# Performance work log

Hardware: AMD Instinct MI355X
Metric: run time of the kernel (lower is better)

Reference implementation:

```python
import jax, jax.numpy as jnp
import numpy as np

N = 16384      # total nodes
B = 8          # graphs in batch
NPG = N // B   # nodes per graph
E = 262144     # edges
IN, HID, OUT = 128, 256, 128
ICP_ITERS = 10


def setup_inputs():
    key = jax.random.key(0)
    ks = jax.random.split(key, 12)
    x = jax.random.normal(ks[0], (N, IN), jnp.float32)
    # random edges kept within each graph (offsets per graph)
    src = jax.random.randint(ks[1], (E,), 0, NPG, dtype=jnp.int32)
    dst = jax.random.randint(ks[2], (E,), 0, NPG, dtype=jnp.int32)
    goff = (jnp.arange(E, dtype=jnp.int32) % B) * NPG
    edge_index = jnp.stack([src + goff, dst + goff], 0)
    pos = jax.random.normal(ks[3], (N, 3), jnp.float32)
    batch = jnp.repeat(jnp.arange(B, dtype=jnp.int32), NPG)
    def lin(k, fi, fo):
        return jax.random.normal(k, (fi, fo), jnp.float32) * (fi ** -0.5)
    return dict(
        x=x, edge_index=edge_index, pos=pos, batch=batch,
        W1=lin(ks[4], IN, HID),  b1=jnp.zeros((HID,), jnp.float32),
        W2=lin(ks[5], HID, HID), b2=jnp.zeros((HID,), jnp.float32),
        W3=lin(ks[6], HID, OUT), b3=jnp.zeros((OUT,), jnp.float32),
        Wt=lin(ks[7], OUT, 3),   bt=jnp.zeros((3,), jnp.float32),
    )


def gcn_conv(x, W, b, row, col, n):
    # GCNConv: symmetric norm with self loops; messages flow row->col
    xw = x @ W
    loop = jnp.arange(n, dtype=row.dtype)
    r = jnp.concatenate([row, loop])
    c = jnp.concatenate([col, loop])
    deg = jax.ops.segment_sum(jnp.ones_like(c, dtype=xw.dtype), c, num_segments=n)
    dinv = jnp.where(deg > 0, jax.lax.rsqrt(jnp.maximum(deg, 1e-12)), 0.0)
    norm = dinv[r] * dinv[c]
    out = jax.ops.segment_sum(xw[r] * norm[:, None], c, num_segments=n)
    return out + b


def pdist2(a, b):
    # squared pairwise distances [n,m]
    return (jnp.sum(a * a, -1)[:, None] + jnp.sum(b * b, -1)[None, :]
            - 2.0 * (a @ b.T))


def icp_align(src, tgt):
    # fixed-iteration batched ICP (Kabsch/SVD per iteration)
    for _ in range(ICP_ITERS):
        d = pdist2(jax.lax.stop_gradient(src), jax.lax.stop_gradient(tgt))
        idx = jnp.argmin(d, axis=1)
        corr = tgt[idx]
        cs = jnp.mean(src, 0)
        cc = jnp.mean(corr, 0)
        H = (src - cs).T @ (corr - cc)  # [3,3]
        U, S, Vt = jnp.linalg.svd(H, full_matrices=False)
        sign = jnp.sign(jnp.linalg.det(Vt.T @ U.T))
        D = jnp.stack([jnp.ones_like(sign), jnp.ones_like(sign), sign])
        R = (Vt.T * D[None, :]) @ U.T
        t = cc - R @ cs
        src = src @ R.T + t
    return src


def chamfer(a, b):
    d = pdist2(jax.lax.stop_gradient(a), jax.lax.stop_gradient(b))
    ia = jnp.argmin(d, 1)
    ib = jnp.argmin(d, 0)
    d1 = jnp.mean(jnp.sum((a - b[ia]) ** 2, -1))
    d2 = jnp.mean(jnp.sum((b - a[ib]) ** 2, -1))
    return d1 + d2


def reference(x, edge_index, pos, batch, W1, b1, W2, b2, W3, b3, Wt, bt):
    n = x.shape[0]
    row, col = edge_index[0], edge_index[1]
    h = jax.nn.relu(gcn_conv(x, W1, b1, row, col, n))
    h = jax.nn.relu(gcn_conv(h, W2, b2, row, col, n))
    h = gcn_conv(h, W3, b3, row, col, n)
    pos_offset = h @ Wt + bt
    tpos = pos + pos_offset
    nb = int(batch[-1]) + 1          # sorted, equal-size graphs
    npg = n // nb
    src = tpos.reshape(nb, npg, 3)
    tgt = pos.reshape(nb, npg, 3)
    aligned = jax.vmap(icp_align)(src, tgt)
    loss = jnp.mean(jax.vmap(chamfer)(aligned, tgt))
    return h, aligned.reshape(n, 3), loss
```

## Files before the change

### kernel.cpp

```cpp
#include <hip/hip_runtime.h>
#include <math.h>

#define N_NODES 16384
#define B_GRAPHS 8
#define NPG_     2048
#define E_EDGES  262144
#define F_IN  128
#define F_HID 256
#define F_OUT 128
#define ICP_IT 10
#define NN_BPG 32

typedef __attribute__((ext_vector_type(8))) short bf16x8;
typedef __attribute__((ext_vector_type(4))) float f32x4;

__device__ __forceinline__ float b2f(unsigned short u) {
    union { unsigned int u; float f; } v; v.u = ((unsigned int)u) << 16; return v.f;
}
__device__ __forceinline__ unsigned short f2b(float f) {
    union { float f; unsigned int u; } v; v.f = f;
    unsigned int r = v.u + 0x7FFFu + ((v.u >> 16) & 1u);
    return (unsigned short)(r >> 16);
}
__device__ __forceinline__ int swz32(int i) {
    return (i & ~31) | ((i & 31) ^ ((i >> 5) & 31));
}
__device__ __forceinline__ void st_agent(float* p, float v) {
    __hip_atomic_store(p, v, __ATOMIC_RELAXED, __HIP_MEMORY_SCOPE_AGENT);
}
__device__ __forceinline__ float ld_agent(const float* p) {
    return __hip_atomic_load(p, __ATOMIC_RELAXED, __HIP_MEMORY_SCOPE_AGENT);
}
__device__ __forceinline__ int ld_agent_i(const int* p) {
    return __hip_atomic_load(p, __ATOMIC_RELAXED, __HIP_MEMORY_SCOPE_AGENT);
}

__global__ __launch_bounds__(256) void k_prep(
    const float* __restrict__ x, unsigned short* __restrict__ xb,
    const float* __restrict__ W1, const float* __restrict__ W2, const float* __restrict__ W3,
    unsigned short* __restrict__ W1b, unsigned short* __restrict__ W2b, unsigned short* __restrict__ W3b,
    int* __restrict__ counts, int* __restrict__ ctrs)
{
    const int b = blockIdx.x, tid = threadIdx.x;
    if (b < 2048) {
        int i = b * 256 + tid;
        float4 v = ((const float4*)x)[i];
        uint2 o;
        o.x = (unsigned int)f2b(v.x) | ((unsigned int)f2b(v.y) << 16);
        o.y = (unsigned int)f2b(v.z) | ((unsigned int)f2b(v.w) << 16);
        ((uint2*)xb)[i] = o;
    } else if (b < 2176) {
        int idx = (b - 2048) * 256 + tid;
        int k = idx >> 8, n = idx & 255;
        W1b[n * 128 + k] = f2b(W1[idx]);
    } else if (b < 2432) {
        int idx = (b - 2176) * 256 + tid;
        int k = idx >> 8, n = idx & 255;
        W2b[n * 256 + k] = f2b(W2[idx]);
    } else if (b < 2560) {
        int idx = (b - 2432) * 256 + tid;
        int k = idx >> 7, n = idx & 127;
        W3b[n * 256 + k] = f2b(W3[idx]);
    } else if (b < 2576) {
        int i = (b - 2560) * 256 + tid;
        ((int4*)counts)[i] = make_int4(0, 0, 0, 0);
    } else {
        ctrs[tid] = 0;
    }
}

__global__ void k_count(const int* __restrict__ col, int* __restrict__ counts) {
    int e = blockIdx.x * 256 + threadIdx.x;
    if (e < E_EDGES) atomicAdd(&counts[col[e]], 1);
}

__global__ __launch_bounds__(1024) void k_scan(const int* __restrict__ counts,
        int* __restrict__ offs, int* __restrict__ cursor, float* __restrict__ dinv)
{
    __shared__ int wtot[16];
    const int t = threadIdx.x;
    const int base = t * 16;
    int local[16];
    int s = 0;
#pragma unroll
    for (int i = 0; i < 16; i++) { local[i] = counts[base + i]; s += local[i]; }
    const int lane = t & 63, w = t >> 6;
    int inc = s;
    for (int o = 1; o < 64; o <<= 1) {
        int v = __shfl_up(inc, o);
        if (lane >= o) inc += v;
    }
    if (lane == 63) wtot[w] = inc;
    __syncthreads();
    if (t < 16) {
        int v = wtot[t];
        for (int o = 1; o < 16; o <<= 1) {
            int u = __shfl_up(v, o);
            if (t >= o) v += u;
        }
        wtot[t] = v;
    }
    __syncthreads();
    int run = (w > 0 ? wtot[w - 1] : 0) + (inc - s);
#pragma unroll
    for (int i = 0; i < 16; i++) {
        offs[base + i]   = run;
        cursor[base + i] = run;
        dinv[base + i]   = rsqrtf((float)(local[i] + 1));
        run += local[i];
    }
    if (t == 1023) offs[N_NODES] = run;
}

__global__ void k_scatter(const int* __restrict__ row, const int* __restrict__ col,
        int* __restrict__ cursor, const float* __restrict__ dinv,
        int* __restrict__ srcid, float* __restrict__ normv)
{
    int e = blockIdx.x * 256 + threadIdx.x;
    if (e >= E_EDGES) return;
    int r = row[e], c = col[e];
    int p = atomicAdd(&cursor[c], 1);
    srcid[p] = r;
    normv[p] = dinv[r] * dinv[c];
}

template<int W, int OUTF, int FUSET>
__global__ __launch_bounds__(128) void k_agg(const unsigned short* __restrict__ X,
        void* __restrict__ Y,
        const int* __restrict__ offs, const int* __restrict__ srcid,
        const float* __restrict__ normv, const float* __restrict__ dinv,
        const float* __restrict__ bias, int relu,
        const float* __restrict__ Wt, const float* __restrict__ bt,
        const float* __restrict__ pos, float* __restrict__ tposO)
{
    constexpr int NPB = (W == 128) ? 2 : 1;
    constexpr int W2 = W / 2;
    const int local = (NPB == 2) ? (threadIdx.x >> 6) : 0;
    const int n = blockIdx.x * NPB + local;
    const int j = (NPB == 2) ? (threadIdx.x & 63) : threadIdx.x;
    const unsigned int* Xu = (const unsigned int*)X;
    float di = dinv[n];
    float w0 = di * di;
    unsigned int v = Xu[(size_t)n * W2 + j];
    float a0 = b2f((unsigned short)v) * w0;
    float a1 = b2f((unsigned short)(v >> 16)) * w0;
    int p = offs[n];
    const int p1 = offs[n + 1];
    for (; p + 3 < p1; p += 4) {
        int s0i = srcid[p], s1i = srcid[p + 1], s2i = srcid[p + 2], s3i = srcid[p + 3];
        float n0 = normv[p], n1 = normv[p + 1], n2 = normv[p + 2], n3 = normv[p + 3];
        unsigned int v0 = Xu[(size_t)s0i * W2 + j];
        unsigned int v1 = Xu[(size_t)s1i * W2 + j];
        unsigned int v2 = Xu[(size_t)s2i * W2 + j];
        unsigned int v3 = Xu[(size_t)s3i * W2 + j];
        a0 = fmaf(b2f((unsigned short)v0), n0, a0);
        a1 = fmaf(b2f((unsigned short)(v0 >> 16)), n0, a1);
        a0 = fmaf(b2f((unsigned short)v1), n1, a0);
        a1 = fmaf(b2f((unsigned short)(v1 >> 16)), n1, a1);
        a0 = fmaf(b2f((unsigned short)v2), n2, a0);
        a1 = fmaf(b2f((unsigned short)(v2 >> 16)), n2, a1);
        a0 = fmaf(b2f((unsigned short)v3), n3, a0);
        a1 = fmaf(b2f((unsigned short)(v3 >> 16)), n3, a1);
    }
    for (; p < p1; ++p) {
        unsigned int va = Xu[(size_t)srcid[p] * W2 + j]; float na = normv[p];
        a0 = fmaf(b2f((unsigned short)va), na, a0);
        a1 = fmaf(b2f((unsigned short)(va >> 16)), na, a1);
    }
    if (bias) { a0 += bias[2 * j]; a1 += bias[2 * j + 1]; }
    if (relu) { a0 = fmaxf(a0, 0.f); a1 = fmaxf(a1, 0.f); }
    if (OUTF) {
        float* Yf = (float*)Y;
        Yf[(size_t)n * W + 2 * j]     = a0;
        Yf[(size_t)n * W + 2 * j + 1] = a1;
    } else {
        ((unsigned int*)Y)[(size_t)n * W2 + j] =
            (unsigned int)f2b(a0) | ((unsigned int)f2b(a1) << 16);
    }
    if (FUSET) {
        float wt0 = Wt[6 * j + 0], wt1 = Wt[6 * j + 1], wt2 = Wt[6 * j + 2];
        float wt3 = Wt[6 * j + 3], wt4 = Wt[6 * j + 4], wt5 = Wt[6 * j + 5];
        float s0 = a0 * wt0 + a1 * wt3;
        float s1 = a0 * wt1 + a1 * wt4;
        float s2 = a0 * wt2 + a1 * wt5;
        for (int o = 32; o > 0; o >>= 1) {
            s0 += __shfl_down(s0, o);
            s1 += __shfl_down(s1, o);
            s2 += __shfl_down(s2, o);
        }
        if (j == 0) {
            tposO[n * 3 + 0] = pos[n * 3 + 0] + s0 + bt[0];
            tposO[n * 3 + 1] = pos[n * 3 + 1] + s1 + bt[1];
            tposO[n * 3 + 2] = pos[n * 3 + 2] + s2 + bt[2];
        }
    }
}

__global__ __launch_bounds__(256) void k_gemm_bf16(
    const unsigned short* __restrict__ A,
    const unsigned short* __restrict__ Bt,
    const float* __restrict__ bias, unsigned short* __restrict__ C,
    int M, int N, int K, int relu)
{
    __shared__ __align__(16) unsigned short As[128 * 64];
    __shared__ __align__(16) unsigned short Bs[64 * 64];
    const int tid  = threadIdx.x;
    const int lane = tid & 63;
    const int wave = tid >> 6;
    const int bm = blockIdx.y * 128, bn = blockIdx.x * 64;
    const int wm = (wave >> 1) * 64, wn = (wave & 1) * 32;
    f32x4 acc[4][2];
#pragma unroll
    for (int mf = 0; mf < 4; mf++)
#pragma unroll
        for (int nf = 0; nf < 2; nf++) acc[mf][nf] = (f32x4){0.f, 0.f, 0.f, 0.f};

    for (int k0 = 0; k0 < K; k0 += 64) {
#pragma unroll
        for (int i = 0; i < 4; i++) {
            int idx = i * 256 + tid;
            int m = idx >> 3, slot = idx & 7;
            const unsigned short* src = A + (size_t)(bm + m) * K + k0 + ((slot ^ (m & 7)) << 3);
            __builtin_amdgcn_global_load_lds(
                (const __attribute__((address_space(1))) unsigned int*)src,
                (__attribute__((address_space(3))) unsigned int*)(As + (size_t)i * 2048 + wave * 512),
                16, 0, 0);
        }
#pragma unroll
        for (int i = 0; i < 2; i++) {
            int idx = i * 256 + tid;
            int n = idx >> 3, slot = idx & 7;
            const unsigned short* src = Bt + (size_t)(bn + n) * K + k0 + ((slot ^ (n & 7)) << 3);
            __builtin_amdgcn_global_load_lds(
                (const __attribute__((address_space(1))) unsigned int*)src,
                (__attribute__((address_space(3))) unsigned int*)(Bs + (size_t)i * 2048 + wave * 512),
                16, 0, 0);
        }
        __syncthreads();
        bf16x8 af[4][2], bfr[2][2];
        const int qd = lane >> 4;
#pragma unroll
        for (int s = 0; s < 2; s++) {
#pragma unroll
            for (int mf = 0; mf < 4; mf++) {
                int m = wm + mf * 16 + (lane & 15);
                int slot = (s * 4 + qd) ^ (m & 7);
                af[mf][s] = *(const bf16x8*)(As + m * 64 + slot * 8);
            }
#pragma unroll
            for (int nf = 0; nf < 2; nf++) {
                int n = wn + nf * 16 + (lane & 15);
                int slot = (s * 4 + qd) ^ (n & 7);
                bfr[nf][s] = *(const bf16x8*)(Bs + n * 64 + slot * 8);
            }
        }
#pragma unroll
        for (int s = 0; s < 2; s++)
#pragma unroll
            for (int mf = 0; mf < 4; mf++)
#pragma unroll
                for (int nf = 0; nf < 2; nf++)
                    acc[mf][nf] = __builtin_amdgcn_mfma_f32_16x16x32_bf16(
                        af[mf][s], bfr[nf][s], acc[mf][nf], 0, 0, 0);
        __syncthreads();
    }
#pragma unroll
    for (int nf = 0; nf < 2; nf++) {
        int col = bn + wn + nf * 16 + (lane & 15);
        float bv = bias ? bias[col] : 0.f;
#pragma unroll
        for (int mf = 0; mf < 4; mf++) {
#pragma unroll
            for (int r = 0; r < 4; r++) {
                int row = bm + wm + mf * 16 + (lane >> 4) * 4 + r;
                float v = acc[mf][nf][r] + bv;
                if (relu) v = fmaxf(v, 0.f);
                C[(size_t)row * N + col] = f2b(v);
            }
        }
    }
}

__global__ __launch_bounds__(512) void k_icp_all(
    const float* __restrict__ tpos, const float* __restrict__ pos,
    float* __restrict__ partials,
    float* __restrict__ chpart,
    int* __restrict__ ctrs,
    float* __restrict__ out_aligned, float* __restrict__ out_loss)
{
    const int g = blockIdx.x >> 5, blk = blockIdx.x & 31;
    const int tid = threadIdx.x;
    const int wave = tid >> 6, lane = tid & 63;
    __shared__ float4 tq[NPG_];
    __shared__ __align__(16) unsigned char scratch[NPG_ * 16];
    float* sm_d = (float*)scratch;
    unsigned short* sm_i = (unsigned short*)(scratch + 64 * 65 * 4);
    float4* al = (float4*)scratch;
    __shared__ float mom[15][33];
    __shared__ float ssx[64], ssy[64], ssz[64];
    __shared__ float wred[16][2];
    __shared__ float Tsh[12];
    __shared__ double sdl[15];
    __shared__ int lastFlag;

    for (int i = tid; i < NPG_; i += 512) {
        const float* p = &pos[(size_t)(g * NPG_ + i) * 3];
        float qx = p[0], qy = p[1], qz = p[2];
        tq[swz32(i)] = make_float4(qx, qy, qz, fmaf(qx, qx, fmaf(qy, qy, qz * qz)));
    }
    if (tid < 12) Tsh[tid] = (tid == 0 || tid == 4 || tid == 8) ? 1.f : 0.f;
    float Px[8], Py[8], Pz[8];
#pragma unroll
    for (int u = 0; u < 8; u++) {
        int n = g * NPG_ + blk * 64 + wave * 8 + u;
        Px[u] = tpos[n * 3 + 0]; Py[u] = tpos[n * 3 + 1]; Pz[u] = tpos[n * 3 + 2];
    }
    double Td[12];
    if (tid == 0) {
#pragma unroll
        for (int k = 0; k < 12; k++) Td[k] = (k == 0 || k == 4 || k == 8) ? 1.0 : 0.0;
    }
    __syncthreads();

    for (int iter = 0; iter < ICP_IT; ++iter) {
        const int bufbase = (iter & 1) * 256;
        float Tf[12];
#pragma unroll
        for (int k = 0; k < 12; k++) Tf[k] = Tsh[k];
        float Sx[8], Sy[8], Sz[8], Tx[8], Ty[8], Tz[8], bd[8];
        int bi[8];
#pragma unroll
        for (int u = 0; u < 8; u++) {
            float X = Tf[0] * Px[u] + Tf[1] * Py[u] + Tf[2] * Pz[u] + Tf[9];
            float Y = Tf[3] * Px[u] + Tf[4] * Py[u] + Tf[5] * Pz[u] + Tf[10];
            float Z = Tf[6] * Px[u] + Tf[7] * Py[u] + Tf[8] * Pz[u] + Tf[11];
            Sx[u] = X; Sy[u] = Y; Sz[u] = Z;
            Tx[u] = -2.f * X; Ty[u] = -2.f * Y; Tz[u] = -2.f * Z;
            bd[u] = 1e30f; bi[u] = lane * 32;
        }
        const int qbase = lane * 32;
        for (int j = 0; j < 32; j++) {
            float4 t4 = tq[qbase + (j ^ (lane & 31))];
            int idx = qbase + j;
#pragma unroll
            for (int u = 0; u < 8; u++) {
                float d = fmaf(Tx[u], t4.x, fmaf(Ty[u], t4.y, fmaf(Tz[u], t4.z, t4.w)));
                if (d < bd[u]) { bd[u] = d; bi[u] = idx; }
            }
        }
#pragma unroll
        for (int u = 0; u < 8; u++) {
            int rowoff = (wave * 8 + u) * 65;
            sm_d[rowoff + lane] = bd[u];
            sm_i[rowoff + lane] = (unsigned short)bi[u];
            if (lane == u) { ssx[wave * 8 + u] = Sx[u]; ssy[wave * 8 + u] = Sy[u]; ssz[wave * 8 + u] = Sz[u]; }
        }
        __syncthreads();
        if (tid < 64) {
            const int s = tid;
            float best = sm_d[s * 65];
            int ib = sm_i[s * 65];
            for (int r = 1; r < 64; r++) {
                float dd = sm_d[s * 65 + r];
                int ii = sm_i[s * 65 + r];
                if (dd < best) { best = dd; ib = ii; }
            }
            float4 c = tq[swz32(ib)];
            float X = ssx[s], Y = ssy[s], Z = ssz[s];
            float vals[15] = { X, Y, Z, c.x, c.y, c.z,
                               X * c.x, X * c.y, X * c.z,
                               Y * c.x, Y * c.y, Y * c.z,
                               Z * c.x, Z * c.y, Z * c.z };
#pragma unroll
            for (int k = 0; k < 15; k++) {
                float v = vals[k];
                for (int o = 32; o > 0; o >>= 1) v += __shfl_down(v, o);
                if (tid == 0) st_agent(&partials[((size_t)bufbase + blockIdx.x) * 16 + k], v);
            }
        }
        __syncthreads();
        if (tid == 0) {
            atomicAdd(&ctrs[g * 16], 1);
            const int target = 32 * (iter + 1);
            while (ld_agent_i(&ctrs[g * 16]) < target) __builtin_amdgcn_s_sleep(8);
        }
        __syncthreads();
        if (tid < 480) {
            int kk = tid >> 5, bb = tid & 31;
            mom[kk][bb] = ld_agent(&partials[((size_t)bufbase + g * 32 + bb) * 16 + kk]);
        }
        __syncthreads();
        if (tid < 15) {
            double acc = 0;
            for (int b = 0; b < NN_BPG; b++) acc += (double)mom[tid][b];
            sdl[tid] = acc;
        }
        __syncthreads();
        if (tid == 0) {
            double sd[15];
#pragma unroll
            for (int k = 0; k < 15; k++) sd[k] = sdl[k];
            const double n = (double)NPG_;
            const double rin = 1.0 / (double)NPG_;
            double cs0 = sd[0] * rin, cs1 = sd[1] * rin, cs2 = sd[2] * rin;
            double cc0 = sd[3] * rin, cc1 = sd[4] * rin, cc2 = sd[5] * rin;
            float H[3][3];
            H[0][0] = (float)(sd[6]  - n * cs0 * cc0); H[0][1] = (float)(sd[7]  - n * cs0 * cc1); H[0][2] = (float)(sd[8]  - n * cs0 * cc2);
            H[1][0] = (float)(sd[9]  - n * cs1 * cc0); H[1][1] = (float)(sd[10] - n * cs1 * cc1); H[1][2] = (float)(sd[11] - n * cs1 * cc2);
            H[2][0] = (float)(sd[12] - n * cs2 * cc0); H[2][1] = (float)(sd[13] - n * cs2 * cc1); H[2][2] = (float)(sd[14] - n * cs2 * cc2);
            double R[3][3];
            float fn = 1e-30f;
            for (int i = 0; i < 3; i++) for (int j2 = 0; j2 < 3; j2++) fn += H[i][j2] * H[i][j2];
            float sc = rsqrtf(fn);
            float Xm[3][3];
            for (int i = 0; i < 3; i++) for (int j2 = 0; j2 < 3; j2++) Xm[i][j2] = H[i][j2] * sc;
            float dX = Xm[0][0] * (Xm[1][1]*Xm[2][2] - Xm[1][2]*Xm[2][1])
                     - Xm[0][1] * (Xm[1][0]*Xm[2][2] - Xm[1][2]*Xm[2][0])
                     + Xm[0][2] * (Xm[1][0]*Xm[2][1] - Xm[1][1]*Xm[2][0]);
            if (dX > 1e-4f) {
                for (int itn = 0; itn < 24; ++itn) {
                    float C00 = Xm[1][1]*Xm[2][2] - Xm[1][2]*Xm[2][1];
                    float C01 = Xm[1][2]*Xm[2][0] - Xm[1][0]*Xm[2][2];
                    float C02 = Xm[1][0]*Xm[2][1] - Xm[1][1]*Xm[2][0];
                    float C10 = Xm[2][1]*Xm[0][2] - Xm[2][2]*Xm[0][1];
                    float C11 = Xm[2][2]*Xm[0][0] - Xm[2][0]*Xm[0][2];
                    float C12 = Xm[2][0]*Xm[0][1] - Xm[2][1]*Xm[0][0];
                    float C20 = Xm[0][1]*Xm[1][2] - Xm[0][2]*Xm[1][1];
                    float C21 = Xm[0][2]*Xm[1][0] - Xm[0][0]*Xm[1][2];
                    float C22 = Xm[0][0]*Xm[1][1] - Xm[0][1]*Xm[1][0];
                    float det = Xm[0][0]*C00 + Xm[0][1]*C01 + Xm[0][2]*C02;
                    if (fabsf(det) < 1e-30f) break;
                    float rd = 0.5f / det;
                    Xm[0][0] = 0.5f*Xm[0][0] + C00*rd; Xm[0][1] = 0.5f*Xm[0][1] + C01*rd; Xm[0][2] = 0.5f*Xm[0][2] + C02*rd;
                    Xm[1][0] = 0.5f*Xm[1][0] + C10*rd; Xm[1][1] = 0.5f*Xm[1][1] + C11*rd; Xm[1][2] = 0.5f*Xm[1][2] + C12*rd;
                    Xm[2][0] = 0.5f*Xm[2][0] + C20*rd; Xm[2][1] = 0.5f*Xm[2][1] + C21*rd; Xm[2][2] = 0.5f*Xm[2][2] + C22*rd;
                }
                for (int i = 0; i < 3; i++) for (int j2 = 0; j2 < 3; j2++) R[i][j2] = (double)Xm[j2][i];
            } else {
                float A[3][3], V[3][3] = {{1,0,0},{0,1,0},{0,0,1}};
                for (int i = 0; i < 3; i++)
                    for (int j2 = 0; j2 < 3; j2++)
                        A[i][j2] = H[0][i] * H[0][j2] + H[1][i] * H[1][j2] + H[2][i] * H[2][j2];
                for (int sweep = 0; sweep < 8; ++sweep) {
                    for (int p = 0; p < 2; p++) for (int q = p + 1; q < 3; q++) {
                        float apq = A[p][q];
                        if (fabsf(apq) < 1e-30f) continue;
                        float theta = (A[q][q] - A[p][p]) / (2.f * apq);
                        float t = copysignf(1.f, theta) / (fabsf(theta) + sqrtf(theta * theta + 1.f));
                        float c = 1.f / sqrtf(t * t + 1.f);
                        float s = t * c;
                        for (int k = 0; k < 3; k++) { float akp = A[k][p], akq = A[k][q]; A[k][p] = c*akp - s*akq; A[k][q] = s*akp + c*akq; }
                        for (int k = 0; k < 3; k++) { float apk = A[p][k], aqk = A[q][k]; A[p][k] = c*apk - s*aqk; A[q][k] = s*apk + c*aqk; }
                        for (int k = 0; k < 3; k++) { float vkp = V[k][p], vkq = V[k][q]; V[k][p] = c*vkp - s*vkq; V[k][q] = s*vkp + c*vkq; }
                    }
                }
                float lam[3] = { A[0][0], A[1][1], A[2][2] };
                int ord[3] = { 0, 1, 2 };
                if (lam[ord[1]] > lam[ord[0]]) { int t0 = ord[0]; ord[0] = ord[1]; ord[1] = t0; }
                if (lam[ord[2]] > lam[ord[0]]) { int t0 = ord[0]; ord[0] = ord[2]; ord[2] = t0; }
                if (lam[ord[2]] > lam[ord[1]]) { int t0 = ord[1]; ord[1] = ord[2]; ord[2] = t0; }
                float vc[3][3], uc[3][3];
                for (int i = 0; i < 3; i++) { vc[i][0] = V[0][ord[i]]; vc[i][1] = V[1][ord[i]]; vc[i][2] = V[2][ord[i]]; }
                for (int i = 0; i < 3; i++) {
                    float u0 = H[0][0]*vc[i][0] + H[0][1]*vc[i][1] + H[0][2]*vc[i][2];
                    float u1 = H[1][0]*vc[i][0] + H[1][1]*vc[i][1] + H[1][2]*vc[i][2];
                    float u2 = H[2][0]*vc[i][0] + H[2][1]*vc[i][1] + H[2][2]*vc[i][2];
                    for (int j2 = 0; j2 < i; j2++) {
                        float dp = u0*uc[j2][0] + u1*uc[j2][1] + u2*uc[j2][2];
                        u0 -= dp*uc[j2][0]; u1 -= dp*uc[j2][1]; u2 -= dp*uc[j2][2];
                    }
                    float nn2 = sqrtf(u0*u0 + u1*u1 + u2*u2);
                    if (nn2 > 1e-12f) { uc[i][0] = u0/nn2; uc[i][1] = u1/nn2; uc[i][2] = u2/nn2; }
                    else if (i == 2) {
                        uc[2][0] = uc[0][1]*uc[1][2] - uc[0][2]*uc[1][1];
                        uc[2][1] = uc[0][2]*uc[1][0] - uc[0][0]*uc[1][2];
                        uc[2][2] = uc[0][0]*uc[1][1] - uc[0][1]*uc[1][0];
                    } else if (i == 1) {
                        float a0 = (fabsf(uc[0][0]) < 0.9f) ? 1.f : 0.f, a1 = 1.f - a0, a2 = 0.f;
                        float dp = a0*uc[0][0] + a1*uc[0][1] + a2*uc[0][2];
                        a0 -= dp*uc[0][0]; a1 -= dp*uc[0][1]; a2 -= dp*uc[0][2];
                        float nn3 = sqrtf(a0*a0 + a1*a1 + a2*a2);
                        uc[1][0] = a0/nn3; uc[1][1] = a1/nn3; uc[1][2] = a2/nn3;
                    } else { uc[0][0] = 1; uc[0][1] = 0; uc[0][2] = 0; }
                }
                float detU = uc[0][0]*(uc[1][1]*uc[2][2] - uc[1][2]*uc[2][1])
                           - uc[0][1]*(uc[1][0]*uc[2][2] - uc[1][2]*uc[2][0])
                           + uc[0][2]*(uc[1][0]*uc[2][1] - uc[1][1]*uc[2][0]);
                float detV = vc[0][0]*(vc[1][1]*vc[2][2] - vc[1][2]*vc[2][1])
                           - vc[0][1]*(vc[1][0]*vc[2][2] - vc[1][2]*vc[2][0])
                           + vc[0][2]*(vc[1][0]*vc[2][1] - vc[1][1]*vc[2][0]);
                float sgn = (detU * detV < 0.f) ? -1.f : 1.f;
                for (int i = 0; i < 3; i++)
                    for (int j2 = 0; j2 < 3; j2++)
                        R[i][j2] = (double)(vc[0][i]*uc[0][j2] + vc[1][i]*uc[1][j2] + sgn * vc[2][i]*uc[2][j2]);
            }
            double tr0 = cc0 - (R[0][0]*cs0 + R[0][1]*cs1 + R[0][2]*cs2);
            double tr1 = cc1 - (R[1][0]*cs0 + R[1][1]*cs1 + R[1][2]*cs2);
            double tr2 = cc2 - (R[2][0]*cs0 + R[2][1]*cs1 + R[2][2]*cs2);
            double An[12];
            for (int i = 0; i < 3; i++)
                for (int j2 = 0; j2 < 3; j2++)
                    An[i*3+j2] = R[i][0]*Td[0*3+j2] + R[i][1]*Td[1*3+j2] + R[i][2]*Td[2*3+j2];
            An[9]  = R[0][0]*Td[9] + R[0][1]*Td[10] + R[0][2]*Td[11] + tr0;
            An[10] = R[1][0]*Td[9] + R[1][1]*Td[10] + R[1][2]*Td[11] + tr1;
            An[11] = R[2][0]*Td[9] + R[2][1]*Td[10] + R[2][2]*Td[11] + tr2;
#pragma unroll
            for (int k = 0; k < 12; k++) { Td[k] = An[k]; Tsh[k] = (float)An[k]; }
        }
        __syncthreads();
    }

    {
        float Tf[12];
#pragma unroll
        for (int k = 0; k < 12; k++) Tf[k] = Tsh[k];
        __syncthreads();
        for (int i = tid; i < NPG_; i += 512) {
            const float* q = &tpos[(size_t)(g * NPG_ + i) * 3];
            float X = Tf[0] * q[0] + Tf[1] * q[1] + Tf[2] * q[2] + Tf[9];
            float Y = Tf[3] * q[0] + Tf[4] * q[1] + Tf[5] * q[2] + Tf[10];
            float Z = Tf[6] * q[0] + Tf[7] * q[1] + Tf[8] * q[2] + Tf[11];
            al[swz32(i)] = make_float4(X, Y, Z, fmaf(X, X, fmaf(Y, Y, Z * Z)));
            if (blk == 0) {
                out_aligned[(size_t)(g * NPG_ + i) * 3 + 0] = X;
                out_aligned[(size_t)(g * NPG_ + i) * 3 + 1] = Y;
                out_aligned[(size_t)(g * NPG_ + i) * 3 + 2] = Z;
            }
        }
        __syncthreads();
        float Ax[8], Ay[8], Az[8], Aw[8], Qx[8], Qy[8], Qz[8], Qw[8], d1[8], d2[8];
#pragma unroll
        for (int u = 0; u < 8; u++) {
            int s = swz32(blk * 64 + wave * 8 + u);
            float4 a4 = al[s]; float4 p4 = tq[s];
            Ax[u] = -2.f * a4.x; Ay[u] = -2.f * a4.y; Az[u] = -2.f * a4.z; Aw[u] = a4.w;
            Qx[u] = -2.f * p4.x; Qy[u] = -2.f * p4.y; Qz[u] = -2.f * p4.z; Qw[u] = p4.w;
            d1[u] = 1e30f; d2[u] = 1e30f;
        }
        const int qbase = lane * 32;
        for (int j = 0; j < 32; j++) {
            int s = qbase + (j ^ (lane & 31));
            float4 t4 = tq[s];
            float4 b4 = al[s];
#pragma unroll
            for (int u = 0; u < 8; u++) {
                d1[u] = fminf(d1[u], fmaf(Ax[u], t4.x, fmaf(Ay[u], t4.y, fmaf(Az[u], t4.z, t4.w))));
                d2[u] = fminf(d2[u], fmaf(Qx[u], b4.x, fmaf(Qy[u], b4.y, fmaf(Qz[u], b4.z, b4.w))));
            }
        }
        float s1 = 0.f, s2 = 0.f;
#pragma unroll
        for (int u = 0; u < 8; u++) {
            float a = d1[u], b = d2[u];
            for (int o = 32; o > 0; o >>= 1) {
                a = fminf(a, __shfl_down(a, o));
                b = fminf(b, __shfl_down(b, o));
            }
            s1 += a + Aw[u];
            s2 += b + Qw[u];
        }
        if (lane == 0) { wred[wave][0] = s1; wred[wave][1] = s2; }
        __syncthreads();
        if (tid == 0) {
            float t1 = 0.f, t2 = 0.f;
#pragma unroll
            for (int w = 0; w < 8; w++) { t1 += wred[w][0]; t2 += wred[w][1]; }
            st_agent(&chpart[blockIdx.x * 2 + 0], t1);
            st_agent(&chpart[blockIdx.x * 2 + 1], t2);
        }
        __syncthreads();
        if (tid == 0) {
            int old = atomicAdd(&ctrs[128], 1);
            lastFlag = (old == (int)gridDim.x - 1) ? 1 : 0;
        }
        __syncthreads();
        if (!lastFlag) return;
        float v1 = 0.f, v2 = 0.f;
        if (tid < 256) {
            v1 = ld_agent(&chpart[tid * 2 + 0]);
            v2 = ld_agent(&chpart[tid * 2 + 1]);
        }
        for (int o = 32; o > 0; o >>= 1) {
            v1 += __shfl_down(v1, o);
            v2 += __shfl_down(v2, o);
        }
        if (lane == 0 && wave < 4) { wred[wave][0] = v1; wred[wave][1] = v2; }
        __syncthreads();
        if (tid == 0) {
            float tot = 0.f;
#pragma unroll
            for (int w = 0; w < 4; w++) tot += wred[w][0] + wred[w][1];
            out_loss[0] = tot / (float)(NPG_ * B_GRAPHS);
        }
    }
}

extern "C" void kernel_launch(void* const* d_in, const int* in_sizes, int n_in,
                              void* d_out, int out_size, void* d_ws, size_t ws_size,
                              hipStream_t stream)
{
    (void)in_sizes; (void)n_in; (void)out_size; (void)ws_size;
    const float* x   = (const float*)d_in[0];
    const int*   ei  = (const int*)d_in[1];
    const float* pos = (const float*)d_in[2];
    const float* W1 = (const float*)d_in[4];
    const float* b1 = (const float*)d_in[5];
    const float* W2 = (const float*)d_in[6];
    const float* b2 = (const float*)d_in[7];
    const float* W3 = (const float*)d_in[8];
    const float* b3 = (const float*)d_in[9];
    const float* Wt = (const float*)d_in[10];
    const float* bt = (const float*)d_in[11];
    const int* row = ei;
    const int* col = ei + E_EDGES;

    char* wsb = (char*)d_ws;
    size_t off_b = 0;
    auto alloc = [&](size_t bytes) -> void* {
        void* p = wsb + off_b;
        off_b = (off_b + bytes + 255) & ~(size_t)255;
        return p;
    };
    int*    counts   = (int*)alloc((size_t)N_NODES * 4);
    int*    offs     = (int*)alloc((size_t)(N_NODES + 1) * 4);
    int*    cursor   = (int*)alloc((size_t)N_NODES * 4);
    int*    srcid    = (int*)alloc((size_t)E_EDGES * 4);
    float*  normv    = (float*)alloc((size_t)E_EDGES * 4);
    float*  dinv     = (float*)alloc((size_t)N_NODES * 4);
    unsigned short* xb  = (unsigned short*)alloc((size_t)N_NODES * F_IN * 2);
    unsigned short* W1b = (unsigned short*)alloc((size_t)F_IN * F_HID * 2);
    unsigned short* W2b = (unsigned short*)alloc((size_t)F_HID * F_HID * 2);
    unsigned short* W3b = (unsigned short*)alloc((size_t)F_HID * F_OUT * 2);
    unsigned short* bufA = (unsigned short*)alloc((size_t)N_NODES * F_HID * 2);
    unsigned short* bufB = (unsigned short*)alloc((size_t)N_NODES * F_HID * 2);
    unsigned short* bufC = (unsigned short*)alloc((size_t)N_NODES * F_HID * 2);
    float*  tpos     = (float*)alloc((size_t)N_NODES * 3 * 4);
    float*  partials = (float*)alloc((size_t)2 * 256 * 16 * 4);
    int*    ctrs     = (int*)alloc((size_t)256 * 4);
    float*  chpart   = (float*)alloc((size_t)256 * 2 * 4);

    float* out_h       = (float*)d_out;
    float* out_aligned = out_h + (size_t)N_NODES * F_OUT;
    float* out_loss    = out_aligned + (size_t)N_NODES * 3;

    k_prep<<<2577, 256, 0, stream>>>(x, xb, W1, W2, W3, W1b, W2b, W3b, counts, ctrs);
    k_count<<<E_EDGES / 256, 256, 0, stream>>>(col, counts);
    k_scan<<<1, 1024, 0, stream>>>(counts, offs, cursor, dinv);
    k_scatter<<<E_EDGES / 256, 256, 0, stream>>>(row, col, cursor, dinv, srcid, normv);

    k_agg<F_IN, 0, 0><<<N_NODES / 2, 128, 0, stream>>>(xb, bufA, offs, srcid, normv, dinv,
            nullptr, 0, nullptr, nullptr, nullptr, nullptr);
    {
        dim3 grid(F_HID / 64, N_NODES / 128);
        k_gemm_bf16<<<grid, 256, 0, stream>>>(bufA, W1b, b1, bufB, N_NODES, F_HID, F_IN, 1);
    }
    {
        dim3 grid(F_HID / 64, N_NODES / 128);
        k_gemm_bf16<<<grid, 256, 0, stream>>>(bufB, W2b, nullptr, bufC, N_NODES, F_HID, F_HID, 0);
    }
    k_agg<F_HID, 0, 0><<<N_NODES, 128, 0, stream>>>(bufC, bufA, offs, srcid, normv, dinv,
            b2, 1, nullptr, nullptr, nullptr, nullptr);
    {
        dim3 grid(F_OUT / 64, N_NODES / 128);
        k_gemm_bf16<<<grid, 256, 0, stream>>>(bufA, W3b, nullptr, bufB, N_NODES, F_OUT, F_HID, 0);
    }
    k_agg<F_OUT, 1, 1><<<N_NODES / 2, 128, 0, stream>>>(bufB, out_h, offs, srcid, normv, dinv,
            b3, 0, Wt, bt, pos, tpos);

    k_icp_all<<<B_GRAPHS * NN_BPG, 512, 0, stream>>>(tpos, pos, partials, chpart, ctrs,
            out_aligned, out_loss);
}
```

Baseline: 330.8 us.

## Split ICP over twice as many smaller blocks and fold edge count into prep

The ICP kernel now runs 512 blocks of 256 threads (64 blocks per graph, 32 source points per block) instead of 256 blocks of 512 threads. The aim is to spread the per-iteration nearest-neighbour search over more compute units, at the cost of a larger cross-block reduction and a grid barrier with more participants each iteration. Separately, the edge-degree counting kernel is merged into the prep kernel, and counts are zeroed by a memset so the standalone count launch goes away. The fused version relies on the memset finishing before prep runs.

```diff
diff --git a/kernel.cpp b/kernel.cpp
--- a/kernel.cpp
+++ b/kernel.cpp
@@ -9,7 +9,6 @@
 #define F_HID 256
 #define F_OUT 128
 #define ICP_IT 10
-#define NN_BPG 32
 
 typedef __attribute__((ext_vector_type(8))) short bf16x8;
 typedef __attribute__((ext_vector_type(4))) float f32x4;
@@ -39,7 +38,7 @@
     const float* __restrict__ x, unsigned short* __restrict__ xb,
     const float* __restrict__ W1, const float* __restrict__ W2, const float* __restrict__ W3,
     unsigned short* __restrict__ W1b, unsigned short* __restrict__ W2b, unsigned short* __restrict__ W3b,
-    int* __restrict__ counts, int* __restrict__ ctrs)
+    const int* __restrict__ col, int* __restrict__ counts, int* __restrict__ ctrs)
 {
     const int b = blockIdx.x, tid = threadIdx.x;
     if (b < 2048) {
@@ -61,17 +60,12 @@
         int idx = (b - 2432) * 256 + tid;
         int k = idx >> 7, n = idx & 127;
         W3b[n * 256 + k] = f2b(W3[idx]);
-    } else if (b < 2576) {
-        int i = (b - 2560) * 256 + tid;
-        ((int4*)counts)[i] = make_int4(0, 0, 0, 0);
+    } else if (b < 3584) {
+        int e = (b - 2560) * 256 + tid;
+        atomicAdd(&counts[col[e]], 1);
     } else {
         ctrs[tid] = 0;
     }
-}
-
-__global__ void k_count(const int* __restrict__ col, int* __restrict__ counts) {
-    int e = blockIdx.x * 256 + threadIdx.x;
-    if (e < E_EDGES) atomicAdd(&counts[col[e]], 1);
 }
 
 __global__ __launch_bounds__(1024) void k_scan(const int* __restrict__ counts,
@@ -281,29 +275,29 @@
     }
 }
 
-__global__ __launch_bounds__(512) void k_icp_all(
+__global__ __launch_bounds__(256, 2) void k_icp_all(
     const float* __restrict__ tpos, const float* __restrict__ pos,
     float* __restrict__ partials,
     float* __restrict__ chpart,
     int* __restrict__ ctrs,
     float* __restrict__ out_aligned, float* __restrict__ out_loss)
 {
-    const int g = blockIdx.x >> 5, blk = blockIdx.x & 31;
+    const int g = blockIdx.x >> 6, blk = blockIdx.x & 63;
     const int tid = threadIdx.x;
     const int wave = tid >> 6, lane = tid & 63;
     __shared__ float4 tq[NPG_];
     __shared__ __align__(16) unsigned char scratch[NPG_ * 16];
     float* sm_d = (float*)scratch;
-    unsigned short* sm_i = (unsigned short*)(scratch + 64 * 65 * 4);
+    unsigned short* sm_i = (unsigned short*)(scratch + 32 * 65 * 4);
     float4* al = (float4*)scratch;
-    __shared__ float mom[15][33];
-    __shared__ float ssx[64], ssy[64], ssz[64];
-    __shared__ float wred[16][2];
+    __shared__ float mom[15][66];
+    __shared__ float crs[32][9];
+    __shared__ float wred[4][2];
     __shared__ float Tsh[12];
     __shared__ double sdl[15];
     __shared__ int lastFlag;
 
-    for (int i = tid; i < NPG_; i += 512) {
+    for (int i = tid; i < NPG_; i += 256) {
         const float* p = &pos[(size_t)(g * NPG_ + i) * 3];
         float qx = p[0], qy = p[1], qz = p[2];
         tq[swz32(i)] = make_float4(qx, qy, qz, fmaf(qx, qx, fmaf(qy, qy, qz * qz)));
@@ -312,7 +306,7 @@
     float Px[8], Py[8], Pz[8];
 #pragma unroll
     for (int u = 0; u < 8; u++) {
-        int n = g * NPG_ + blk * 64 + wave * 8 + u;
+        int n = g * NPG_ + blk * 32 + wave * 8 + u;
         Px[u] = tpos[n * 3 + 0]; Py[u] = tpos[n * 3 + 1]; Pz[u] = tpos[n * 3 + 2];
     }
     double Td[12];
@@ -323,7 +317,7 @@
     __syncthreads();
 
     for (int iter = 0; iter < ICP_IT; ++iter) {
-        const int bufbase = (iter & 1) * 256;
+        const int bufbase = (iter & 1) * 512;
         float Tf[12];
 #pragma unroll
         for (int k = 0; k < 12; k++) Tf[k] = Tsh[k];
@@ -350,49 +344,56 @@
         }
 #pragma unroll
         for (int u = 0; u < 8; u++) {
-            int rowoff = (wave * 8 + u) * 65;
-            sm_d[rowoff + lane] = bd[u];
-            sm_i[rowoff + lane] = (unsigned short)bi[u];
-            if (lane == u) { ssx[wave * 8 + u] = Sx[u]; ssy[wave * 8 + u] = Sy[u]; ssz[wave * 8 + u] = Sz[u]; }
-        }
-        __syncthreads();
-        if (tid < 64) {
-            const int s = tid;
-            float best = sm_d[s * 65];
-            int ib = sm_i[s * 65];
+            int row = wave * 8 + u;
+            sm_d[row * 65 + lane] = bd[u];
+            sm_i[row * 65 + lane] = (unsigned short)bi[u];
+            if (lane == u) { crs[row][0] = Sx[u]; crs[row][1] = Sy[u]; crs[row][2] = Sz[u]; }
+        }
+        __syncthreads();
+        if (tid < 32) {
+            float best = sm_d[tid * 65];
+            int ib = sm_i[tid * 65];
             for (int r = 1; r < 64; r++) {
-                float dd = sm_d[s * 65 + r];
-                int ii = sm_i[s * 65 + r];
+                float dd = sm_d[tid * 65 + r];
+                int ii = sm_i[tid * 65 + r];
                 if (dd < best) { best = dd; ib = ii; }
             }
             float4 c = tq[swz32(ib)];
-            float X = ssx[s], Y = ssy[s], Z = ssz[s];
-            float vals[15] = { X, Y, Z, c.x, c.y, c.z,
-                               X * c.x, X * c.y, X * c.z,
-                               Y * c.x, Y * c.y, Y * c.z,
-                               Z * c.x, Z * c.y, Z * c.z };
+            crs[tid][3] = c.x; crs[tid][4] = c.y; crs[tid][5] = c.z;
+        }
+        __syncthreads();
+        if (wave == 0) {
+            float X = 0.f, Y = 0.f, Z = 0.f, cx = 0.f, cy = 0.f, cz = 0.f;
+            if (lane < 32) {
+                X = crs[lane][0]; Y = crs[lane][1]; Z = crs[lane][2];
+                cx = crs[lane][3]; cy = crs[lane][4]; cz = crs[lane][5];
+            }
+            float vals[15] = { X, Y, Z, cx, cy, cz,
+                               X * cx, X * cy, X * cz,
+                               Y * cx, Y * cy, Y * cz,
+                               Z * cx, Z * cy, Z * cz };
 #pragma unroll
             for (int k = 0; k < 15; k++) {
                 float v = vals[k];
                 for (int o = 32; o > 0; o >>= 1) v += __shfl_down(v, o);
-                if (tid == 0) st_agent(&partials[((size_t)bufbase + blockIdx.x) * 16 + k], v);
+                if (lane == 0) st_agent(&partials[((size_t)bufbase + blockIdx.x) * 16 + k], v);
             }
         }
         __syncthreads();
         if (tid == 0) {
-            atomicAdd(&ctrs[g * 16], 1);
-            const int target = 32 * (iter + 1);
-            while (ld_agent_i(&ctrs[g * 16]) < target) __builtin_amdgcn_s_sleep(8);
-        }
-        __syncthreads();
-        if (tid < 480) {
-            int kk = tid >> 5, bb = tid & 31;
-            mom[kk][bb] = ld_agent(&partials[((size_t)bufbase + g * 32 + bb) * 16 + kk]);
+            atomicAdd(&ctrs[g * 32], 1);
+            const int target = 64 * (iter + 1);
+            while (ld_agent_i(&ctrs[g * 32]) < target) __builtin_amdgcn_s_sleep(2);
+        }
+        __syncthreads();
+        for (int idx = tid; idx < 960; idx += 256) {
+            int kk = idx >> 6, bb = idx & 63;
+            mom[kk][bb] = ld_agent(&partials[((size_t)bufbase + g * 64 + bb) * 16 + kk]);
         }
         __syncthreads();
         if (tid < 15) {
             double acc = 0;
-            for (int b = 0; b < NN_BPG; b++) acc += (double)mom[tid][b];
+            for (int b = 0; b < 64; b++) acc += (double)mom[tid][b];
             sdl[tid] = acc;
         }
         __syncthreads();
@@ -515,7 +516,7 @@
 #pragma unroll
         for (int k = 0; k < 12; k++) Tf[k] = Tsh[k];
         __syncthreads();
-        for (int i = tid; i < NPG_; i += 512) {
+        for (int i = tid; i < NPG_; i += 256) {
             const float* q = &tpos[(size_t)(g * NPG_ + i) * 3];
             float X = Tf[0] * q[0] + Tf[1] * q[1] + Tf[2] * q[2] + Tf[9];
             float Y = Tf[3] * q[0] + Tf[4] * q[1] + Tf[5] * q[2] + Tf[10];
@@ -531,7 +532,7 @@
         float Ax[8], Ay[8], Az[8], Aw[8], Qx[8], Qy[8], Qz[8], Qw[8], d1[8], d2[8];
 #pragma unroll
         for (int u = 0; u < 8; u++) {
-            int s = swz32(blk * 64 + wave * 8 + u);
+            int s = swz32(blk * 32 + wave * 8 + u);
             float4 a4 = al[s]; float4 p4 = tq[s];
             Ax[u] = -2.f * a4.x; Ay[u] = -2.f * a4.y; Az[u] = -2.f * a4.z; Aw[u] = a4.w;
             Qx[u] = -2.f * p4.x; Qy[u] = -2.f * p4.y; Qz[u] = -2.f * p4.z; Qw[u] = p4.w;
@@ -564,27 +565,24 @@
         if (tid == 0) {
             float t1 = 0.f, t2 = 0.f;
 #pragma unroll
-            for (int w = 0; w < 8; w++) { t1 += wred[w][0]; t2 += wred[w][1]; }
+            for (int w = 0; w < 4; w++) { t1 += wred[w][0]; t2 += wred[w][1]; }
             st_agent(&chpart[blockIdx.x * 2 + 0], t1);
             st_agent(&chpart[blockIdx.x * 2 + 1], t2);
         }
         __syncthreads();
         if (tid == 0) {
-            int old = atomicAdd(&ctrs[128], 1);
+            int old = atomicAdd(&ctrs[255], 1);
             lastFlag = (old == (int)gridDim.x - 1) ? 1 : 0;
         }
         __syncthreads();
         if (!lastFlag) return;
-        float v1 = 0.f, v2 = 0.f;
-        if (tid < 256) {
-            v1 = ld_agent(&chpart[tid * 2 + 0]);
-            v2 = ld_agent(&chpart[tid * 2 + 1]);
-        }
+        float v1 = ld_agent(&chpart[tid * 2 + 0]) + ld_agent(&chpart[(tid + 256) * 2 + 0]);
+        float v2 = ld_agent(&chpart[tid * 2 + 1]) + ld_agent(&chpart[(tid + 256) * 2 + 1]);
         for (int o = 32; o > 0; o >>= 1) {
             v1 += __shfl_down(v1, o);
             v2 += __shfl_down(v2, o);
         }
-        if (lane == 0 && wave < 4) { wred[wave][0] = v1; wred[wave][1] = v2; }
+        if (lane == 0) { wred[wave][0] = v1; wred[wave][1] = v2; }
         __syncthreads();
         if (tid == 0) {
             float tot = 0.f;
@@ -635,16 +633,16 @@
     unsigned short* bufB = (unsigned short*)alloc((size_t)N_NODES * F_HID * 2);
     unsigned short* bufC = (unsigned short*)alloc((size_t)N_NODES * F_HID * 2);
     float*  tpos     = (float*)alloc((size_t)N_NODES * 3 * 4);
-    float*  partials = (float*)alloc((size_t)2 * 256 * 16 * 4);
+    float*  partials = (float*)alloc((size_t)2 * 512 * 16 * 4);
     int*    ctrs     = (int*)alloc((size_t)256 * 4);
-    float*  chpart   = (float*)alloc((size_t)256 * 2 * 4);
+    float*  chpart   = (float*)alloc((size_t)512 * 2 * 4);
 
     float* out_h       = (float*)d_out;
     float* out_aligned = out_h + (size_t)N_NODES * F_OUT;
     float* out_loss    = out_aligned + (size_t)N_NODES * 3;
 
-    k_prep<<<2577, 256, 0, stream>>>(x, xb, W1, W2, W3, W1b, W2b, W3b, counts, ctrs);
-    k_count<<<E_EDGES / 256, 256, 0, stream>>>(col, counts);
+    hipMemsetAsync(counts, 0, (size_t)N_NODES * 4, stream);
+    k_prep<<<3585, 256, 0, stream>>>(x, xb, W1, W2, W3, W1b, W2b, W3b, col, counts, ctrs);
     k_scan<<<1, 1024, 0, stream>>>(counts, offs, cursor, dinv);
     k_scatter<<<E_EDGES / 256, 256, 0, stream>>>(row, col, cursor, dinv, srcid, normv);
 
@@ -667,6 +665,6 @@
     k_agg<F_OUT, 1, 1><<<N_NODES / 2, 128, 0, stream>>>(bufB, out_h, offs, srcid, normv, dinv,
             b3, 0, Wt, bt, pos, tpos);
 
-    k_icp_all<<<B_GRAPHS * NN_BPG, 512, 0, stream>>>(tpos, pos, partials, chpart, ctrs,
+    k_icp_all<<<512, 256, 0, stream>>>(tpos, pos, partials, chpart, ctrs,
             out_aligned, out_loss);
 }
```

New measurement: 357.1 us. 8.0% more time.
